# Performance work log

Hardware: AMD Instinct MI355X
Metric: run time of the kernel (lower is better)

## Reference

```python
import jax, jax.numpy as jnp
import numpy as np

WINDOW = 3
RATIO = 5


def _box_filter(x, win):
    """Depthwise 3D box (mean) filter, 'same' padding, per channel.
    x: [N, C, D, H, W] -> [N, C, D, H, W]
    Matches torch conv3d with ones([1,1,w,w,w])/w^3 applied per channel.
    """
    c = x.shape[1]
    k = jnp.ones((c, 1, win, win, win), x.dtype) / (win ** 3)
    pad = win // 2
    return jax.lax.conv_general_dilated(
        x, k,
        window_strides=(1, 1, 1),
        padding=[(pad, pad)] * 3,
        dimension_numbers=('NCDHW', 'OIDHW', 'NCDHW'),
        feature_group_count=c,
    )


def setup_inputs() -> dict:
    key = jax.random.key(0)
    k1, k2 = jax.random.split(key)
    y_pred = jax.random.normal(k1, (1, 3, 192, 192, 192), dtype=jnp.float32)
    y_true = jax.random.uniform(k2, (1, 1, 192, 192, 192), dtype=jnp.float32)
    return {"y_pred": y_pred, "y_true": y_true}


def reference(y_pred, y_true):
    # Finite differences (abs), each [1, 3, D-1, H-1, W-1]
    base = y_pred[:, :, :-1, :-1, :-1]
    dy = jnp.abs(y_pred[:, :, 1:, :-1, :-1] - base)
    dx = jnp.abs(y_pred[:, :, :-1, 1:, :-1] - base)
    dz = jnp.abs(y_pred[:, :, :-1, :-1, 1:] - base)

    # 9 box-filtered single-channel maps == 3 depthwise box filters
    fx = _box_filter(dx, WINDOW)
    fy = _box_filter(dy, WINDOW)
    fz = _box_filter(dz, WINDOW)
    dxdx, dxdy, dxdz = fx[:, 1:2], fy[:, 1:2], fz[:, 1:2]
    dydx, dydy, dydz = fx[:, 0:1], fy[:, 0:1], fz[:, 0:1]
    dzdx, dzdy, dzdz = fx[:, 2:3], fy[:, 2:3], fz[:, 2:3]

    # Neo-Hookean invariants
    det_1 = (dxdx + 1) * ((dydy + 1) * (dzdz + 1) - dydz * dzdy)
    det_2 = -dxdy * (dydx * (dzdz + 1) - dydz * dzdx)
    det_3 = dxdz * (dydx * dzdy - (dydy + 1) * dzdx)
    J = det_1 + det_2 + det_3

    Tr = ((dxdx + 1) ** 2 + dxdy ** 2 + dxdz ** 2
          + dydx ** 2 + (dydy + 1) ** 2 + dydz ** 2
          + dzdx ** 2 + dzdy ** 2 + (dzdz + 1) ** 2)

    # mode == 'exp'
    stretch = Tr * jnp.exp(-J + 1) - 3
    vol_change = (J - 1) ** 2

    # Faithful replication of the sequential mu/lambda normalization in torch:
    mu = 1.0
    lam = mu * RATIO
    mu = mu / (mu + lam)          # 1/6
    lam = lam / (mu + lam)        # 30/31 (uses updated mu, as in source)

    U = mu / 2 * stretch + lam / 2 * vol_change
    return jnp.mean(U)
```

## Files before the change

### kernel.cpp

```cpp
#include <hip/hip_runtime.h>
#include <math.h>

#define DIM 192
#define OD  191
#define PLANE 36864
#define VOL 7077888
#define TW  14
#define TH  16
#define CD  16
#define NBW 14
#define NBH 12
#define NCH 12

typedef float    f4 __attribute__((ext_vector_type(4)));
typedef _Float16 h8 __attribute__((ext_vector_type(8)));
typedef _Float16 h4 __attribute__((ext_vector_type(4)));
typedef _Float16 h2 __attribute__((ext_vector_type(2)));

template<int CTRL>
__device__ __forceinline__ int dppi(int x) {
    return __builtin_amdgcn_update_dpp(0, x, CTRL, 0xF, 0xF, true);
}

union U8 { h8 v; int i[4]; };
union U2 { h2 v; int i; };

__device__ __forceinline__ void wsum3(h8& a, h2& b) {
    U8 ua, s1, s2;
    ua.v = a;
    #pragma unroll
    for (int k = 0; k < 4; ++k) {
        s1.i[k] = dppi<0x101>(ua.i[k]);
        s2.i[k] = dppi<0x111>(ua.i[k]);
    }
    a = ua.v + s1.v + s2.v;
    U2 ub, t1, t2;
    ub.v = b;
    t1.i = dppi<0x101>(ub.i);
    t2.i = dppi<0x111>(ub.i);
    b = ub.v + t1.v + t2.v;
}

__device__ __forceinline__ void make_diff16(const h4 c, const h4 cw, const h4 ch, const h4 cd,
                                            h8& va, h2& vb) {
    const h4 dh = __builtin_elementwise_abs(ch - c);
    const h4 dd = __builtin_elementwise_abs(cd - c);
    const h4 dw = __builtin_elementwise_abs(cw - c);
    va = (h8){dh[0], dh[1], dh[2], dd[0], dd[1], dd[2], dw[0], dw[1]};
    vb = (h2){dw[2], (_Float16)0.f};
}

__device__ __forceinline__ f4 ld3(const float* __restrict__ P, int idx, bool ok) {
    f4 r = (f4)0;
    if (ok) {
        r.x = P[idx];
        r.y = P[idx + VOL];
        r.z = P[idx + 2 * VOL];
    }
    return r;
}

__device__ __forceinline__ h4 cvt16(const f4 v) {
    return (h4){(_Float16)v.x, (_Float16)v.y, (_Float16)v.z, (_Float16)0.f};
}

__global__ __launch_bounds__(256, 8)
void nh_fused_kernel(const float* __restrict__ P, float* __restrict__ out) {
    const int tid = threadIdx.x;
    const int tx  = tid & 15;
    const int ty  = tid >> 4;
    const int w0  = blockIdx.x * TW;
    const int h0  = blockIdx.y * TH;
    const int ds  = blockIdx.z * CD;
    const int de  = min(ds + CD, OD);

    __shared__ h4 sraw[2][19][18];
    __shared__ h8 sW[2][18][16];
    __shared__ h2 sWB[2][18][16];
    __shared__ float wsum[4];

    const int hp_p = h0 - 1 + ty;
    const int wp_p = w0 - 1 + tx;
    const bool in_raw_p  = (hp_p >= 0) & (hp_p < DIM) & (wp_p >= 0) & (wp_p < DIM);
    const bool in_diff_p = (hp_p >= 0) & (hp_p < OD)  & (wp_p >= 0) & (wp_p < OD);
    const int base_p = hp_p * DIM + wp_p;

    int hh_l, ww_l;
    if (tid < 48) { hh_l = 16 + (tid >> 4); ww_l = tid & 15; }
    else          { hh_l = tid - 48;        ww_l = 16; }
    const bool has_l = (tid < 67);
    const int hp_l = h0 - 1 + hh_l;
    const int wp_l = w0 - 1 + ww_l;
    const bool in_raw_l  = has_l & (hp_l >= 0) & (hp_l < DIM) & (wp_l >= 0) & (wp_l < DIM);
    const bool in_diff_l = (tid < 32) & (hp_l >= 0) & (hp_l < OD) & (wp_l >= 0) & (wp_l < OD);
    const int base_l = hp_l * DIM + wp_l;

    const bool valid = (tx < TW) && (w0 + tx < OD) && (h0 + ty < OD);

    h8 a0 = (h8)0, a1 = (h8)0, a2 = (h8)0;
    h2 b0 = (h2)0, b1 = (h2)0, b2 = (h2)0;
    f4 cur_p = (f4)0, cur_l = (f4)0;
    h4 prev16_p = (h4)0, prev16_l = (h4)0;
    float acc = 0.f;

    {
        const int t0 = ds - 1;
        if (t0 >= 0) {
            cur_p = ld3(P, t0 * PLANE + base_p, in_raw_p);
            cur_l = ld3(P, t0 * PLANE + base_l, in_raw_l);
        }
    }

    for (int t = ds - 1; t <= de + 1; ++t) {
        const int cb = t & 1, pb = cb ^ 1;

        f4 nxt_p = (f4)0, nxt_l = (f4)0;
        {
            const int tn = t + 1;
            if ((tn < DIM) & (tn <= de + 1)) {
                nxt_p = ld3(P, tn * PLANE + base_p, in_raw_p);
                nxt_l = ld3(P, tn * PLANE + base_l, in_raw_l);
            }
        }

        const h4 cur16_p = cvt16(cur_p);
        sraw[cb][ty][tx] = cur16_p;
        h4 cur16_l = (h4)0;
        if (has_l) {
            cur16_l = cvt16(cur_l);
            sraw[cb][hh_l][ww_l] = cur16_l;
        }

        const bool built = (t >= ds) & (t - 1 >= 0) & (t - 1 < OD);

        {
            h8 sa = (h8)0; h2 sb = (h2)0;
            if (built) {
                h8 va = (h8)0; h2 vb = (h2)0;
                if (in_diff_p) {
                    make_diff16(prev16_p,
                                sraw[pb][ty][tx + 1],
                                sraw[pb][ty + 1][tx],
                                cur16_p, va, vb);
                }
                wsum3(va, vb);
                sa = va; sb = vb;
            }
            sW[cb][ty][tx] = sa; sWB[cb][ty][tx] = sb;
        }
        if (tid < 32) {
            h8 sa = (h8)0; h2 sb = (h2)0;
            if (built) {
                h8 va = (h8)0; h2 vb = (h2)0;
                if (in_diff_l) {
                    make_diff16(prev16_l,
                                sraw[pb][hh_l][ww_l + 1],
                                sraw[pb][hh_l + 1][ww_l],
                                cur16_l, va, vb);
                }
                wsum3(va, vb);
                sa = va; sb = vb;
            }
            sW[cb][hh_l][ww_l] = sa; sWB[cb][hh_l][ww_l] = sb;
        }

        __syncthreads();

        a0 = a1; a1 = a2; b0 = b1; b1 = b2;
        {
            const int cc = (tx + 1) & 15;
            a2 = sW[cb][ty][cc] + sW[cb][ty + 1][cc] + sW[cb][ty + 2][cc];
            b2 = sWB[cb][ty][cc] + sWB[cb][ty + 1][cc] + sWB[cb][ty + 2][cc];
        }

        const int d = t - 2;
        if (valid && d >= ds && d < de) {
            const h8 FA = a0 + a1 + a2;
            const h2 FB = b0 + b1 + b2;
            const float inv27 = 1.f / 27.f;
            const float dydx = (float)FA[0] * inv27, dxdx = (float)FA[1] * inv27, dzdx = (float)FA[2] * inv27;
            const float dydy = (float)FA[3] * inv27, dxdy = (float)FA[4] * inv27, dzdy = (float)FA[5] * inv27;
            const float dydz = (float)FA[6] * inv27, dxdz = (float)FA[7] * inv27, dzdz = (float)FB[0] * inv27;
            const float a = dxdx + 1.f, e = dydy + 1.f, iN = dzdz + 1.f;
            const float J = a * (e * iN - dydz * dzdy)
                          - dxdy * (dydx * iN - dydz * dzdx)
                          + dxdz * (dydx * dzdy - e * dzdx);
            const float Tr = a * a + dxdy * dxdy + dxdz * dxdz
                           + dydx * dydx + e * e + dydz * dydz
                           + dzdx * dzdx + dzdy * dzdy + iN * iN;
            const float stretch = Tr * __expf(1.f - J) - 3.f;
            const float vol = (J - 1.f) * (J - 1.f);
            acc += 0.0833333358f * stretch + 0.4838709677f * vol;
        }

        prev16_p = cur16_p; cur_p = nxt_p;
        prev16_l = cur16_l; cur_l = nxt_l;
    }

    acc *= (1.f / 6967871.f);

    #pragma unroll
    for (int off = 32; off > 0; off >>= 1) acc += __shfl_down(acc, off, 64);
    if ((tid & 63) == 0) wsum[tid >> 6] = acc;
    __syncthreads();
    if (tid == 0) {
        atomicAdd(out, wsum[0] + wsum[1] + wsum[2] + wsum[3]);
    }
}

extern "C" void kernel_launch(void* const* d_in, const int* in_sizes, int n_in,
                              void* d_out, int out_size, void* d_ws, size_t ws_size,
                              hipStream_t stream) {
    const float* y_pred = (const float*)d_in[0];
    float* out = (float*)d_out;

    hipMemsetAsync(out, 0, sizeof(float), stream);

    dim3 grid(NBW, NBH, NCH);
    nh_fused_kernel<<<grid, 256, 0, stream>>>(y_pred, out);
}
```

Baseline: 172.6 us.

## Compute two H rows per thread with 32-row tiles and packed float2 energy math

Each thread now handles two output rows (ty and ty+16) of a 32-row tile, which halves the halo overhead in H per block. Depth chunks shrink to 12 and the grid becomes 14x6x16. The energy evaluation is done on float2 vectors so the compiler can emit packed FP32 ops, and validity masks replace the branch. The cost is more registers per thread, hence launch bounds dropping from 8 to 5 waves, and larger shared memory per block, which may reduce occupancy and latency hiding.

```diff
diff --git a/kernel.cpp b/kernel.cpp
--- a/kernel.cpp
+++ b/kernel.cpp
@@ -6,13 +6,14 @@
 #define PLANE 36864
 #define VOL 7077888
 #define TW  14
-#define TH  16
-#define CD  16
+#define TH  32
+#define CD  12
 #define NBW 14
-#define NBH 12
-#define NCH 12
+#define NBH 6
+#define NCH 16
 
 typedef float    f4 __attribute__((ext_vector_type(4)));
+typedef float    f2 __attribute__((ext_vector_type(2)));
 typedef _Float16 h8 __attribute__((ext_vector_type(8)));
 typedef _Float16 h4 __attribute__((ext_vector_type(4)));
 typedef _Float16 h2 __attribute__((ext_vector_type(2)));
@@ -64,7 +65,30 @@
     return (h4){(_Float16)v.x, (_Float16)v.y, (_Float16)v.z, (_Float16)0.f};
 }
 
-__global__ __launch_bounds__(256, 8)
+__device__ __forceinline__ f2 energy2(const h8 FAa, const h2 FBa,
+                                      const h8 FAb, const h2 FBb) {
+    const float inv27 = 1.f / 27.f;
+#define MK2(i) ((f2){(float)FAa[i], (float)FAb[i]} * inv27)
+    const f2 dydx = MK2(0), dxdx = MK2(1), dzdx = MK2(2);
+    const f2 dydy = MK2(3), dxdy = MK2(4), dzdy = MK2(5);
+    const f2 dydz = MK2(6), dxdz = MK2(7);
+#undef MK2
+    const f2 dzdz = (f2){(float)FBa[0], (float)FBb[0]} * inv27;
+    const f2 a = dxdx + 1.f, e = dydy + 1.f, iN = dzdz + 1.f;
+    const f2 J = a * (e * iN - dydz * dzdy)
+               - dxdy * (dydx * iN - dydz * dzdx)
+               + dxdz * (dydx * dzdy - e * dzdx);
+    const f2 Tr = a * a + dxdy * dxdy + dxdz * dxdz
+                + dydx * dydx + e * e + dydz * dydz
+                + dzdx * dzdx + dzdy * dzdy + iN * iN;
+    const f2 ex = (f2){__expf(1.f - J.x), __expf(1.f - J.y)};
+    const f2 stretch = Tr * ex - 3.f;
+    const f2 jm1 = J - 1.f;
+    const f2 vol = jm1 * jm1;
+    return 0.0833333358f * stretch + 0.4838709677f * vol;
+}
+
+__global__ __launch_bounds__(256, 5)
 void nh_fused_kernel(const float* __restrict__ P, float* __restrict__ out) {
     const int tid = threadIdx.x;
     const int tx  = tid & 15;
@@ -74,89 +98,116 @@
     const int ds  = blockIdx.z * CD;
     const int de  = min(ds + CD, OD);
 
-    __shared__ h4 sraw[2][19][18];
-    __shared__ h8 sW[2][18][16];
-    __shared__ h2 sWB[2][18][16];
+    __shared__ h4 sraw[2][35][18];
+    __shared__ h8 sW[2][34][16];
+    __shared__ h2 sWB[2][34][16];
     __shared__ float wsum[4];
 
-    const int hp_p = h0 - 1 + ty;
-    const int wp_p = w0 - 1 + tx;
-    const bool in_raw_p  = (hp_p >= 0) & (hp_p < DIM) & (wp_p >= 0) & (wp_p < DIM);
-    const bool in_diff_p = (hp_p >= 0) & (hp_p < OD)  & (wp_p >= 0) & (wp_p < OD);
-    const int base_p = hp_p * DIM + wp_p;
-
-    int hh_l, ww_l;
-    if (tid < 48) { hh_l = 16 + (tid >> 4); ww_l = tid & 15; }
-    else          { hh_l = tid - 48;        ww_l = 16; }
-    const bool has_l = (tid < 67);
+    const int wp = w0 - 1 + tx;
+    const bool wr = (wp >= 0) & (wp < DIM);
+    const bool wd = (wp >= 0) & (wp < OD);
+
+    const int hpA = h0 - 1 + ty;
+    const int hpB = hpA + 16;
+    const bool in_raw_A  = wr & (hpA >= 0) & (hpA < DIM);
+    const bool in_raw_B  = wr & (hpB < DIM);
+    const bool in_diff_A = wd & (hpA >= 0) & (hpA < OD);
+    const bool in_diff_B = wd & (hpB < OD);
+    const int baseA = hpA * DIM + wp;
+    const int baseB = hpB * DIM + wp;
+
+    int hh_l = 0, ww_l = 0;
+    bool has_l = false;
+    if (tid < 48)      { hh_l = 32 + (tid >> 4); ww_l = tid & 15; has_l = true; }
+    else if (tid < 83) { hh_l = tid - 48;        ww_l = 16;       has_l = true; }
     const int hp_l = h0 - 1 + hh_l;
     const int wp_l = w0 - 1 + ww_l;
     const bool in_raw_l  = has_l & (hp_l >= 0) & (hp_l < DIM) & (wp_l >= 0) & (wp_l < DIM);
     const bool in_diff_l = (tid < 32) & (hp_l >= 0) & (hp_l < OD) & (wp_l >= 0) & (wp_l < OD);
     const int base_l = hp_l * DIM + wp_l;
 
-    const bool valid = (tx < TW) && (w0 + tx < OD) && (h0 + ty < OD);
-
-    h8 a0 = (h8)0, a1 = (h8)0, a2 = (h8)0;
-    h2 b0 = (h2)0, b1 = (h2)0, b2 = (h2)0;
-    f4 cur_p = (f4)0, cur_l = (f4)0;
-    h4 prev16_p = (h4)0, prev16_l = (h4)0;
-    float acc = 0.f;
+    const bool validA = (tx < TW) && (w0 + tx < OD) && (h0 + ty < OD);
+    const bool validB = (tx < TW) && (w0 + tx < OD) && (h0 + ty + 16 < OD);
+
+    h8 aA0 = (h8)0, aA1 = (h8)0, aA2 = (h8)0, aB0 = (h8)0, aB1 = (h8)0, aB2 = (h8)0;
+    h2 bA0 = (h2)0, bA1 = (h2)0, bA2 = (h2)0, bB0 = (h2)0, bB1 = (h2)0, bB2 = (h2)0;
+    f4 curA = (f4)0, curB = (f4)0, curL = (f4)0;
+    h4 prevA = (h4)0, prevB = (h4)0, prevL = (h4)0;
+    f2 acc = (f2)0;
 
     {
         const int t0 = ds - 1;
         if (t0 >= 0) {
-            cur_p = ld3(P, t0 * PLANE + base_p, in_raw_p);
-            cur_l = ld3(P, t0 * PLANE + base_l, in_raw_l);
+            curA = ld3(P, t0 * PLANE + baseA, in_raw_A);
+            curB = ld3(P, t0 * PLANE + baseB, in_raw_B);
+            curL = ld3(P, t0 * PLANE + base_l, in_raw_l);
         }
     }
 
     for (int t = ds - 1; t <= de + 1; ++t) {
         const int cb = t & 1, pb = cb ^ 1;
 
-        f4 nxt_p = (f4)0, nxt_l = (f4)0;
+        f4 nxtA = (f4)0, nxtB = (f4)0, nxtL = (f4)0;
         {
             const int tn = t + 1;
             if ((tn < DIM) & (tn <= de + 1)) {
-                nxt_p = ld3(P, tn * PLANE + base_p, in_raw_p);
-                nxt_l = ld3(P, tn * PLANE + base_l, in_raw_l);
-            }
-        }
-
-        const h4 cur16_p = cvt16(cur_p);
-        sraw[cb][ty][tx] = cur16_p;
-        h4 cur16_l = (h4)0;
+                nxtA = ld3(P, tn * PLANE + baseA, in_raw_A);
+                nxtB = ld3(P, tn * PLANE + baseB, in_raw_B);
+                nxtL = ld3(P, tn * PLANE + base_l, in_raw_l);
+            }
+        }
+
+        const h4 c16A = cvt16(curA);
+        const h4 c16B = cvt16(curB);
+        sraw[cb][ty][tx]      = c16A;
+        sraw[cb][ty + 16][tx] = c16B;
+        h4 c16L = (h4)0;
         if (has_l) {
-            cur16_l = cvt16(cur_l);
-            sraw[cb][hh_l][ww_l] = cur16_l;
-        }
-
-        const bool built = (t >= ds) & (t - 1 >= 0) & (t - 1 < OD);
+            c16L = cvt16(curL);
+            sraw[cb][hh_l][ww_l] = c16L;
+        }
+
+        const bool built = (t >= ds) & (t - 1 >= 0);
 
         {
             h8 sa = (h8)0; h2 sb = (h2)0;
             if (built) {
                 h8 va = (h8)0; h2 vb = (h2)0;
-                if (in_diff_p) {
-                    make_diff16(prev16_p,
+                if (in_diff_A) {
+                    make_diff16(prevA,
                                 sraw[pb][ty][tx + 1],
                                 sraw[pb][ty + 1][tx],
-                                cur16_p, va, vb);
+                                c16A, va, vb);
                 }
                 wsum3(va, vb);
                 sa = va; sb = vb;
             }
             sW[cb][ty][tx] = sa; sWB[cb][ty][tx] = sb;
+        }
+        {
+            h8 sa = (h8)0; h2 sb = (h2)0;
+            if (built) {
+                h8 va = (h8)0; h2 vb = (h2)0;
+                if (in_diff_B) {
+                    make_diff16(prevB,
+                                sraw[pb][ty + 16][tx + 1],
+                                sraw[pb][ty + 17][tx],
+                                c16B, va, vb);
+                }
+                wsum3(va, vb);
+                sa = va; sb = vb;
+            }
+            sW[cb][ty + 16][tx] = sa; sWB[cb][ty + 16][tx] = sb;
         }
         if (tid < 32) {
             h8 sa = (h8)0; h2 sb = (h2)0;
             if (built) {
                 h8 va = (h8)0; h2 vb = (h2)0;
                 if (in_diff_l) {
-                    make_diff16(prev16_l,
+                    make_diff16(prevL,
                                 sraw[pb][hh_l][ww_l + 1],
                                 sraw[pb][hh_l + 1][ww_l],
-                                cur16_l, va, vb);
+                                c16L, va, vb);
                 }
                 wsum3(va, vb);
                 sa = va; sb = vb;
@@ -166,42 +217,37 @@
 
         __syncthreads();
 
-        a0 = a1; a1 = a2; b0 = b1; b1 = b2;
+        aA0 = aA1; aA1 = aA2; bA0 = bA1; bA1 = bA2;
+        aB0 = aB1; aB1 = aB2; bB0 = bB1; bB1 = bB2;
         {
             const int cc = (tx + 1) & 15;
-            a2 = sW[cb][ty][cc] + sW[cb][ty + 1][cc] + sW[cb][ty + 2][cc];
-            b2 = sWB[cb][ty][cc] + sWB[cb][ty + 1][cc] + sWB[cb][ty + 2][cc];
+            aA2 = sW[cb][ty][cc]      + sW[cb][ty + 1][cc]  + sW[cb][ty + 2][cc];
+            bA2 = sWB[cb][ty][cc]     + sWB[cb][ty + 1][cc] + sWB[cb][ty + 2][cc];
+            aB2 = sW[cb][ty + 16][cc] + sW[cb][ty + 17][cc] + sW[cb][ty + 18][cc];
+            bB2 = sWB[cb][ty + 16][cc]+ sWB[cb][ty + 17][cc]+ sWB[cb][ty + 18][cc];
         }
 
         const int d = t - 2;
-        if (valid && d >= ds && d < de) {
-            const h8 FA = a0 + a1 + a2;
-            const h2 FB = b0 + b1 + b2;
-            const float inv27 = 1.f / 27.f;
-            const float dydx = (float)FA[0] * inv27, dxdx = (float)FA[1] * inv27, dzdx = (float)FA[2] * inv27;
-            const float dydy = (float)FA[3] * inv27, dxdy = (float)FA[4] * inv27, dzdy = (float)FA[5] * inv27;
-            const float dydz = (float)FA[6] * inv27, dxdz = (float)FA[7] * inv27, dzdz = (float)FB[0] * inv27;
-            const float a = dxdx + 1.f, e = dydy + 1.f, iN = dzdz + 1.f;
-            const float J = a * (e * iN - dydz * dzdy)
-                          - dxdy * (dydx * iN - dydz * dzdx)
-                          + dxdz * (dydx * dzdy - e * dzdx);
-            const float Tr = a * a + dxdy * dxdy + dxdz * dxdz
-                           + dydx * dydx + e * e + dydz * dydz
-                           + dzdx * dzdx + dzdy * dzdy + iN * iN;
-            const float stretch = Tr * __expf(1.f - J) - 3.f;
-            const float vol = (J - 1.f) * (J - 1.f);
-            acc += 0.0833333358f * stretch + 0.4838709677f * vol;
-        }
-
-        prev16_p = cur16_p; cur_p = nxt_p;
-        prev16_l = cur16_l; cur_l = nxt_l;
-    }
-
-    acc *= (1.f / 6967871.f);
+        if (d >= ds && d < de) {
+            const h8 FAa = aA0 + aA1 + aA2;
+            const h2 FBa = bA0 + bA1 + bA2;
+            const h8 FAb = aB0 + aB1 + aB2;
+            const h2 FBb = bB0 + bB1 + bB2;
+            const f2 u = energy2(FAa, FBa, FAb, FBb);
+            acc.x += validA ? u.x : 0.f;
+            acc.y += validB ? u.y : 0.f;
+        }
+
+        prevA = c16A; curA = nxtA;
+        prevB = c16B; curB = nxtB;
+        prevL = c16L; curL = nxtL;
+    }
+
+    float accs = (acc.x + acc.y) * (1.f / 6967871.f);
 
     #pragma unroll
-    for (int off = 32; off > 0; off >>= 1) acc += __shfl_down(acc, off, 64);
-    if ((tid & 63) == 0) wsum[tid >> 6] = acc;
+    for (int off = 32; off > 0; off >>= 1) accs += __shfl_down(accs, off, 64);
+    if ((tid & 63) == 0) wsum[tid >> 6] = accs;
     __syncthreads();
     if (tid == 0) {
         atomicAdd(out, wsum[0] + wsum[1] + wsum[2] + wsum[3]);
```

Result: slower. 176.2 us (+2.1%).
